# Optimization experiments

Hardware: AMD Instinct MI355X
Metric: run time of the kernel (lower is better)

The kernel has to match this reference:

```python
import jax, jax.numpy as jnp
import numpy as np

ALPHA = 0.2  # LeakyReLU slope
NEG_BIG = -9e15


def setup_inputs() -> dict:
    key = jax.random.key(0)
    ks = jax.random.split(key, 6)
    N, F_IN, F_OUT, F_E = 8192, 256, 64, 8
    h = jax.random.normal(ks[0], (N, F_IN), dtype=jnp.float32)
    edge = jax.random.normal(ks[1], (N, F_E), dtype=jnp.float32)
    adj = jax.random.randint(ks[2], (N, N), 0, 2, dtype=jnp.int32)
    W = jax.random.normal(ks[3], (F_IN, F_OUT), dtype=jnp.float32) * 0.09  # ~xavier
    a = jax.random.normal(ks[4], (3 * F_OUT, 1), dtype=jnp.float32) * 0.12
    We = jax.random.normal(ks[5], (F_E, F_OUT), dtype=jnp.float32) * 0.28
    return {"h": h, "edge": edge, "adj": adj, "W": W, "a": a, "We": We}


def reference(h, edge, adj, W, a, We):
    F_OUT = W.shape[1]
    Wh = h @ W                      # [N, F]
    WeE = edge @ We                 # [N, F]
    a1 = a[:F_OUT, 0]               # source term
    a2 = a[F_OUT:2 * F_OUT, 0]      # target term
    a3 = a[2 * F_OUT:, 0]           # edge (source-indexed) term
    # e[i, j] = leakyrelu(Wh[i].a1 + Wh[j].a2 + WeE[i].a3)  == original repeat/cat @ a
    src = Wh @ a1 + WeE @ a3        # [N]
    dst = Wh @ a2                   # [N]
    e = jax.nn.leaky_relu(src[:, None] + dst[None, :], negative_slope=ALPHA)
    scores = jnp.where(adj > 0, e, NEG_BIG)
    attention = jax.nn.softmax(scores, axis=1)  # dropout p=0.0 / eval: identity
    h_prime = attention @ Wh        # [N, F]
    return jax.nn.elu(h_prime)      # concat=True
```

## Files before the change

### kernel.cpp

```cpp
#include <hip/hip_runtime.h>

typedef float v4f __attribute__((ext_vector_type(4)));
typedef short v8s __attribute__((ext_vector_type(8)));

#define ALPHA 0.2f
#define LOG2E 1.44269504088896340736f
#define NROW 8192
#define FIN 256
#define FOUT 64
#define JSPLIT 8
#define JCHUNK (NROW / JSPLIT)
#define NSTEP (JCHUNK / 32)

static __device__ __forceinline__ unsigned short f2bf(float f) {
  unsigned int u = __builtin_bit_cast(unsigned int, f);
  u += 0x7fff + ((u >> 16) & 1);
  return (unsigned short)(u >> 16);
}
static __device__ __forceinline__ float bf2f(unsigned short s) {
  unsigned int u = ((unsigned int)s) << 16;
  return __builtin_bit_cast(float, u);
}

__global__ __launch_bounds__(256) void k1_proj(
    const float* __restrict__ h, const float* __restrict__ edge,
    const float* __restrict__ W, const float* __restrict__ a,
    const float* __restrict__ We, unsigned short* __restrict__ whT,
    float* __restrict__ srcv, float* __restrict__ dstv) {
  __shared__ float Ws[FIN * FOUT];
  int tid = threadIdx.x;
  const float4* Wg = (const float4*)W;
  float4* Wl = (float4*)Ws;
#pragma unroll
  for (int it = 0; it < 16; ++it) Wl[it * 256 + tid] = Wg[it * 256 + tid];
  int lane = tid & 63;
  int wave = tid >> 6;
  float a1c = a[lane], a2c = a[64 + lane], a3c = a[128 + lane];
  float Wer[8];
#pragma unroll
  for (int k = 0; k < 8; ++k) Wer[k] = We[k * 64 + lane];
  __syncthreads();
  int rbase = blockIdx.x * 16 + wave * 4;
  const float* hr0 = h + (long)(rbase + 0) * FIN;
  const float* hr1 = h + (long)(rbase + 1) * FIN;
  const float* hr2 = h + (long)(rbase + 2) * FIN;
  const float* hr3 = h + (long)(rbase + 3) * FIN;
  float acc0 = 0.f, acc1 = 0.f, acc2 = 0.f, acc3 = 0.f;
#pragma unroll 2
  for (int k = 0; k < FIN; k += 4) {
    float4 h0 = *(const float4*)(hr0 + k);
    float4 h1 = *(const float4*)(hr1 + k);
    float4 h2 = *(const float4*)(hr2 + k);
    float4 h3 = *(const float4*)(hr3 + k);
#pragma unroll
    for (int t = 0; t < 4; ++t) {
      float w = Ws[(k + t) * 64 + lane];
      float e0 = (t == 0) ? h0.x : (t == 1) ? h0.y : (t == 2) ? h0.z : h0.w;
      float e1 = (t == 0) ? h1.x : (t == 1) ? h1.y : (t == 2) ? h1.z : h1.w;
      float e2 = (t == 0) ? h2.x : (t == 1) ? h2.y : (t == 2) ? h2.z : h2.w;
      float e3 = (t == 0) ? h3.x : (t == 1) ? h3.y : (t == 2) ? h3.z : h3.w;
      acc0 = __builtin_fmaf(e0, w, acc0);
      acc1 = __builtin_fmaf(e1, w, acc1);
      acc2 = __builtin_fmaf(e2, w, acc2);
      acc3 = __builtin_fmaf(e3, w, acc3);
    }
  }
#pragma unroll
  for (int rr = 0; rr < 4; ++rr) {
    int r = rbase + rr;
    float acc = (rr == 0) ? acc0 : (rr == 1) ? acc1 : (rr == 2) ? acc2 : acc3;
    float4 e0 = *(const float4*)(edge + r * 8);
    float4 e1 = *(const float4*)(edge + r * 8 + 4);
    float aedge = e0.x * Wer[0] + e0.y * Wer[1] + e0.z * Wer[2] +
                  e0.w * Wer[3] + e1.x * Wer[4] + e1.y * Wer[5] +
                  e1.z * Wer[6] + e1.w * Wer[7];
    float ps = acc * a1c + aedge * a3c;
    float pd = acc * a2c;
#pragma unroll
    for (int off = 32; off >= 1; off >>= 1) {
      ps += __shfl_xor(ps, off);
      pd += __shfl_xor(pd, off);
    }
    whT[((long)(r >> 5)) * 2048 + lane * 32 + (r & 31)] = f2bf(acc);
    if (lane == 0) {
      srcv[r] = ps;
      dstv[r] = pd;
    }
  }
}

__global__ __launch_bounds__(256) void k1b_dstmax(const float* __restrict__ dstv,
                                                  float* __restrict__ dmax) {
  int tid = threadIdx.x;
  float m = -1e30f;
  for (int k = tid; k < NROW; k += 256) m = fmaxf(m, dstv[k]);
#pragma unroll
  for (int off = 32; off >= 1; off >>= 1) m = fmaxf(m, __shfl_xor(m, off));
  __shared__ float red[4];
  if ((tid & 63) == 0) red[tid >> 6] = m;
  __syncthreads();
  if (tid == 0) dmax[0] = fmaxf(fmaxf(red[0], red[1]), fmaxf(red[2], red[3]));
}

struct AdjB {
  int4 a0, a1;
};
struct DWB {
  float4 d0, d1;
  v8s b0, b1, b2, b3;
};

static __device__ __forceinline__ void adjload(AdjB& A,
                                               const int* __restrict__ adj,
                                               long rowbase, int g, int jj) {
  const int* ap = adj + rowbase + jj + g * 8;
  A.a0 = *(const int4*)ap;
  A.a1 = *(const int4*)(ap + 4);
}

static __device__ __forceinline__ void dwload(DWB& D,
                                              const float* __restrict__ dstv,
                                              const unsigned short* __restrict__ whT,
                                              int g, int m, int jj) {
  const float* dp = dstv + jj + g * 8;
  D.d0 = *(const float4*)dp;
  D.d1 = *(const float4*)(dp + 4);
  const unsigned short* wp = whT + ((long)(jj >> 5)) * 2048 + m * 32 + g * 8;
  D.b0 = *(const v8s*)(wp + 0);
  D.b1 = *(const v8s*)(wp + 512);
  D.b2 = *(const v8s*)(wp + 1024);
  D.b3 = *(const v8s*)(wp + 1536);
}

static __device__ __forceinline__ void computestep(const AdjB& A, const DWB& D,
                                                   float sv, float M2, v4f& a0,
                                                   v4f& a1, v4f& a2, v4f& a3,
                                                   float& ssum) {
  v8s aw;
#define WCALC(adji, dsti, slot)                                 \
  {                                                             \
    float x = sv + (dsti);                                      \
    float lr = fmaxf(x, ALPHA * x);                             \
    float w = exp2f(__builtin_fmaf(lr, LOG2E, -M2));            \
    unsigned short wb = ((adji) > 0) ? f2bf(w) : (unsigned short)0; \
    ssum += bf2f(wb);                                           \
    aw[slot] = (short)wb;                                       \
  }
  WCALC(A.a0.x, D.d0.x, 0)
  WCALC(A.a0.y, D.d0.y, 1)
  WCALC(A.a0.z, D.d0.z, 2)
  WCALC(A.a0.w, D.d0.w, 3)
  WCALC(A.a1.x, D.d1.x, 4)
  WCALC(A.a1.y, D.d1.y, 5)
  WCALC(A.a1.z, D.d1.z, 6)
  WCALC(A.a1.w, D.d1.w, 7)
#undef WCALC
  a0 = __builtin_amdgcn_mfma_f32_16x16x32_bf16(aw, D.b0, a0, 0, 0, 0);
  a1 = __builtin_amdgcn_mfma_f32_16x16x32_bf16(aw, D.b1, a1, 0, 0, 0);
  a2 = __builtin_amdgcn_mfma_f32_16x16x32_bf16(aw, D.b2, a2, 0, 0, 0);
  a3 = __builtin_amdgcn_mfma_f32_16x16x32_bf16(aw, D.b3, a3, 0, 0, 0);
}

__global__ __launch_bounds__(256) void k2_attn(
    const int* __restrict__ adj, const float* __restrict__ srcg,
    const float* __restrict__ dstv, const float* __restrict__ dmax,
    const unsigned short* __restrict__ whT, float* __restrict__ hpart,
    float* __restrict__ spart) {
  int tid = threadIdx.x;
  int lane = tid & 63;
  int wave = tid >> 6;
  int rtile = blockIdx.x * 64 + wave * 16;
  int jy = blockIdx.y;
  int jbase = jy * JCHUNK;
  int m = lane & 15;
  int g = lane >> 4;
  int row = rtile + m;
  long rowbase = (long)row * NROW;
  float sv = srcg[row];
  float dm = dmax[0];
  float xm = sv + dm;
  float M2 = fmaxf(xm, ALPHA * xm) * LOG2E;
  v4f a0 = {}, a1 = {}, a2 = {}, a3 = {};
  float ssum = 0.f;
  AdjB A0, A1;
  DWB D0, D1;
  adjload(A0, adj, rowbase, g, jbase + 0 * 32);
  adjload(A1, adj, rowbase, g, jbase + 1 * 32);
  dwload(D0, dstv, whT, g, m, jbase + 0 * 32);
  for (int t = 0; t < NSTEP; t += 2) {
    dwload(D1, dstv, whT, g, m, jbase + (t + 1) * 32);
    computestep(A0, D0, sv, M2, a0, a1, a2, a3, ssum);
    if (t + 2 < NSTEP) {
      adjload(A0, adj, rowbase, g, jbase + (t + 2) * 32);
      dwload(D0, dstv, whT, g, m, jbase + (t + 2) * 32);
    }
    computestep(A1, D1, sv, M2, a0, a1, a2, a3, ssum);
    if (t + 3 < NSTEP)
      adjload(A1, adj, rowbase, g, jbase + (t + 3) * 32);
  }
  ssum += __shfl_xor(ssum, 16);
  ssum += __shfl_xor(ssum, 32);
  if (g == 0) spart[jy * NROW + row] = ssum;
  float* hp = hpart + ((long)jy * NROW + rtile) * FOUT;
#pragma unroll
  for (int r = 0; r < 4; ++r) {
    hp[(g * 4 + r) * FOUT + 0 + m] = a0[r];
    hp[(g * 4 + r) * FOUT + 16 + m] = a1[r];
    hp[(g * 4 + r) * FOUT + 32 + m] = a2[r];
    hp[(g * 4 + r) * FOUT + 48 + m] = a3[r];
  }
}

__global__ __launch_bounds__(256) void k3_fin(const float* __restrict__ hpart,
                                              const float* __restrict__ spart,
                                              float* __restrict__ out) {
  long g4 = (long)blockIdx.x * 256 + threadIdx.x;
  long base = g4 * 4;
  int i = (int)(base >> 6);
  float4 num = {0.f, 0.f, 0.f, 0.f};
  float den = 0.f;
#pragma unroll
  for (int p = 0; p < JSPLIT; ++p) {
    float4 v = *(const float4*)(hpart + (long)p * NROW * FOUT + base);
    num.x += v.x;
    num.y += v.y;
    num.z += v.z;
    num.w += v.w;
    den += spart[p * NROW + i];
  }
  float rd = 1.0f / den;
  float4 o;
  o.x = num.x * rd;
  o.y = num.y * rd;
  o.z = num.z * rd;
  o.w = num.w * rd;
  o.x = o.x > 0.f ? o.x : (__expf(o.x) - 1.0f);
  o.y = o.y > 0.f ? o.y : (__expf(o.y) - 1.0f);
  o.z = o.z > 0.f ? o.z : (__expf(o.z) - 1.0f);
  o.w = o.w > 0.f ? o.w : (__expf(o.w) - 1.0f);
  *(float4*)(out + base) = o;
}

extern "C" void kernel_launch(void* const* d_in, const int* in_sizes, int n_in,
                              void* d_out, int out_size, void* d_ws,
                              size_t ws_size, hipStream_t stream) {
  const float* h = (const float*)d_in[0];
  const float* edge = (const float*)d_in[1];
  const int* adj = (const int*)d_in[2];
  const float* W = (const float*)d_in[3];
  const float* a = (const float*)d_in[4];
  const float* We = (const float*)d_in[5];
  float* out = (float*)d_out;
  char* ws = (char*)d_ws;
  unsigned short* whT = (unsigned short*)ws;
  float* srcv = (float*)(ws + 1048576);
  float* dstv = (float*)(ws + 1081344);
  float* dmax = (float*)(ws + 1114112);
  float* spart = (float*)(ws + 1114368);
  float* hpart = (float*)(ws + 1376512);
  hipLaunchKernelGGL(k1_proj, dim3(512), dim3(256), 0, stream, h, edge, W, a,
                     We, whT, srcv, dstv);
  hipLaunchKernelGGL(k1b_dstmax, dim3(1), dim3(256), 0, stream, dstv, dmax);
  hipLaunchKernelGGL(k2_attn, dim3(128, JSPLIT), dim3(256), 0, stream, adj,
                     srcv, dstv, dmax, whT, hpart, spart);
  hipLaunchKernelGGL(k3_fin, dim3(512), dim3(256), 0, stream, hpart, spart,
                     out);
}
```

Before: 452.5 us.

## Split columns across waves in-block and fuse final reduction into attention kernel

```diff
diff --git a/kernel.cpp b/kernel.cpp
--- a/kernel.cpp
+++ b/kernel.cpp
@@ -2,15 +2,15 @@
 
 typedef float v4f __attribute__((ext_vector_type(4)));
 typedef short v8s __attribute__((ext_vector_type(8)));
+typedef int v4i __attribute__((ext_vector_type(4)));
 
 #define ALPHA 0.2f
 #define LOG2E 1.44269504088896340736f
 #define NROW 8192
 #define FIN 256
 #define FOUT 64
-#define JSPLIT 8
-#define JCHUNK (NROW / JSPLIT)
-#define NSTEP (JCHUNK / 32)
+#define COLS_PER_WAVE 2048
+#define NSTEP2 (COLS_PER_WAVE / 32)
 
 static __device__ __forceinline__ unsigned short f2bf(float f) {
   unsigned int u = __builtin_bit_cast(unsigned int, f);
@@ -103,7 +103,7 @@
 }
 
 struct AdjB {
-  int4 a0, a1;
+  v4i a0, a1;
 };
 struct DWB {
   float4 d0, d1;
@@ -113,9 +113,9 @@
 static __device__ __forceinline__ void adjload(AdjB& A,
                                                const int* __restrict__ adj,
                                                long rowbase, int g, int jj) {
-  const int* ap = adj + rowbase + jj + g * 8;
-  A.a0 = *(const int4*)ap;
-  A.a1 = *(const int4*)(ap + 4);
+  const v4i* ap = (const v4i*)(adj + rowbase + jj + g * 8);
+  A.a0 = __builtin_nontemporal_load(ap);
+  A.a1 = __builtin_nontemporal_load(ap + 1);
 }
 
 static __device__ __forceinline__ void dwload(DWB& D,
@@ -146,14 +146,14 @@
     ssum += bf2f(wb);                                           \
     aw[slot] = (short)wb;                                       \
   }
-  WCALC(A.a0.x, D.d0.x, 0)
-  WCALC(A.a0.y, D.d0.y, 1)
-  WCALC(A.a0.z, D.d0.z, 2)
-  WCALC(A.a0.w, D.d0.w, 3)
-  WCALC(A.a1.x, D.d1.x, 4)
-  WCALC(A.a1.y, D.d1.y, 5)
-  WCALC(A.a1.z, D.d1.z, 6)
-  WCALC(A.a1.w, D.d1.w, 7)
+  WCALC(A.a0[0], D.d0.x, 0)
+  WCALC(A.a0[1], D.d0.y, 1)
+  WCALC(A.a0[2], D.d0.z, 2)
+  WCALC(A.a0[3], D.d0.w, 3)
+  WCALC(A.a1[0], D.d1.x, 4)
+  WCALC(A.a1[1], D.d1.y, 5)
+  WCALC(A.a1[2], D.d1.z, 6)
+  WCALC(A.a1[3], D.d1.w, 7)
 #undef WCALC
   a0 = __builtin_amdgcn_mfma_f32_16x16x32_bf16(aw, D.b0, a0, 0, 0, 0);
   a1 = __builtin_amdgcn_mfma_f32_16x16x32_bf16(aw, D.b1, a1, 0, 0, 0);
@@ -164,14 +164,14 @@
 __global__ __launch_bounds__(256) void k2_attn(
     const int* __restrict__ adj, const float* __restrict__ srcg,
     const float* __restrict__ dstv, const float* __restrict__ dmax,
-    const unsigned short* __restrict__ whT, float* __restrict__ hpart,
-    float* __restrict__ spart) {
+    const unsigned short* __restrict__ whT, float* __restrict__ out) {
+  __shared__ float nums[4][16][68];
+  __shared__ float dens[4][16];
   int tid = threadIdx.x;
   int lane = tid & 63;
   int wave = tid >> 6;
-  int rtile = blockIdx.x * 64 + wave * 16;
-  int jy = blockIdx.y;
-  int jbase = jy * JCHUNK;
+  int rtile = blockIdx.x * 16;
+  int jbase = wave * COLS_PER_WAVE;
   int m = lane & 15;
   int g = lane >> 4;
   int row = rtile + m;
@@ -187,58 +187,52 @@
   adjload(A0, adj, rowbase, g, jbase + 0 * 32);
   adjload(A1, adj, rowbase, g, jbase + 1 * 32);
   dwload(D0, dstv, whT, g, m, jbase + 0 * 32);
-  for (int t = 0; t < NSTEP; t += 2) {
+  for (int t = 0; t < NSTEP2; t += 2) {
     dwload(D1, dstv, whT, g, m, jbase + (t + 1) * 32);
     computestep(A0, D0, sv, M2, a0, a1, a2, a3, ssum);
-    if (t + 2 < NSTEP) {
+    if (t + 2 < NSTEP2) {
       adjload(A0, adj, rowbase, g, jbase + (t + 2) * 32);
       dwload(D0, dstv, whT, g, m, jbase + (t + 2) * 32);
     }
     computestep(A1, D1, sv, M2, a0, a1, a2, a3, ssum);
-    if (t + 3 < NSTEP)
+    if (t + 3 < NSTEP2)
       adjload(A1, adj, rowbase, g, jbase + (t + 3) * 32);
   }
   ssum += __shfl_xor(ssum, 16);
   ssum += __shfl_xor(ssum, 32);
-  if (g == 0) spart[jy * NROW + row] = ssum;
-  float* hp = hpart + ((long)jy * NROW + rtile) * FOUT;
+  if (g == 0) dens[wave][m] = ssum;
 #pragma unroll
   for (int r = 0; r < 4; ++r) {
-    hp[(g * 4 + r) * FOUT + 0 + m] = a0[r];
-    hp[(g * 4 + r) * FOUT + 16 + m] = a1[r];
-    hp[(g * 4 + r) * FOUT + 32 + m] = a2[r];
-    hp[(g * 4 + r) * FOUT + 48 + m] = a3[r];
-  }
-}
-
-__global__ __launch_bounds__(256) void k3_fin(const float* __restrict__ hpart,
-                                              const float* __restrict__ spart,
-                                              float* __restrict__ out) {
-  long g4 = (long)blockIdx.x * 256 + threadIdx.x;
-  long base = g4 * 4;
-  int i = (int)(base >> 6);
-  float4 num = {0.f, 0.f, 0.f, 0.f};
+    nums[wave][g * 4 + r][0 + m] = a0[r];
+    nums[wave][g * 4 + r][16 + m] = a1[r];
+    nums[wave][g * 4 + r][32 + m] = a2[r];
+    nums[wave][g * 4 + r][48 + m] = a3[r];
+  }
+  __syncthreads();
+  int orow = tid >> 4;
+  int ocol = (tid & 15) * 4;
+  float4 n = {0.f, 0.f, 0.f, 0.f};
   float den = 0.f;
 #pragma unroll
-  for (int p = 0; p < JSPLIT; ++p) {
-    float4 v = *(const float4*)(hpart + (long)p * NROW * FOUT + base);
-    num.x += v.x;
-    num.y += v.y;
-    num.z += v.z;
-    num.w += v.w;
-    den += spart[p * NROW + i];
+  for (int w = 0; w < 4; ++w) {
+    float4 v = *(const float4*)&nums[w][orow][ocol];
+    n.x += v.x;
+    n.y += v.y;
+    n.z += v.z;
+    n.w += v.w;
+    den += dens[w][orow];
   }
   float rd = 1.0f / den;
   float4 o;
-  o.x = num.x * rd;
-  o.y = num.y * rd;
-  o.z = num.z * rd;
-  o.w = num.w * rd;
+  o.x = n.x * rd;
+  o.y = n.y * rd;
+  o.z = n.z * rd;
+  o.w = n.w * rd;
   o.x = o.x > 0.f ? o.x : (__expf(o.x) - 1.0f);
   o.y = o.y > 0.f ? o.y : (__expf(o.y) - 1.0f);
   o.z = o.z > 0.f ? o.z : (__expf(o.z) - 1.0f);
   o.w = o.w > 0.f ? o.w : (__expf(o.w) - 1.0f);
-  *(float4*)(out + base) = o;
+  *(float4*)(out + (long)(rtile + orow) * FOUT + ocol) = o;
 }
 
 extern "C" void kernel_launch(void* const* d_in, const int* in_sizes, int n_in,
@@ -256,13 +250,9 @@
   float* srcv = (float*)(ws + 1048576);
   float* dstv = (float*)(ws + 1081344);
   float* dmax = (float*)(ws + 1114112);
-  float* spart = (float*)(ws + 1114368);
-  float* hpart = (float*)(ws + 1376512);
   hipLaunchKernelGGL(k1_proj, dim3(512), dim3(256), 0, stream, h, edge, W, a,
                      We, whT, srcv, dstv);
   hipLaunchKernelGGL(k1b_dstmax, dim3(1), dim3(256), 0, stream, dstv, dmax);
-  hipLaunchKernelGGL(k2_attn, dim3(128, JSPLIT), dim3(256), 0, stream, adj,
-                     srcv, dstv, dmax, whT, hpart, spart);
-  hipLaunchKernelGGL(k3_fin, dim3(512), dim3(256), 0, stream, hpart, spart,
-                     out);
-}
+  hipLaunchKernelGGL(k2_attn, dim3(512), dim3(256), 0, stream, adj, srcv, dstv,
+                     dmax, whT, out);
+}
```

Result: faster. 419.1 us (-7.4%).
